# Performance work log

Hardware: AMD Instinct MI355X
Metric: run time of the kernel (lower is better)

Reference implementation:

```python
import jax, jax.numpy as jnp
import numpy as np

N_NODES = 100000
IN_C, HID_C, OUT_C = 128, 64, 16
N_EDGES = 3200000


def gcn_conv(x, W, b, src, dst, deg_inv_sqrt, n_nodes):
    """PyG GCNConv: out = D^-1/2 (A+I) D^-1/2 (x @ W) + b.
    src/dst already include self-loops; deg_inv_sqrt precomputed."""
    h = x @ W  # [N, out_c]
    norm = deg_inv_sqrt[src] * deg_inv_sqrt[dst]  # [E+N]
    msg = h[src] * norm[:, None]                  # gather + scale
    out = jax.ops.segment_sum(msg, dst, num_segments=n_nodes)
    return out + b


def _prep_edges(edge_index, n_nodes):
    loops = jnp.arange(n_nodes, dtype=edge_index.dtype)
    src = jnp.concatenate([edge_index[0], loops])
    dst = jnp.concatenate([edge_index[1], loops])
    deg = jax.ops.segment_sum(jnp.ones_like(dst, dtype=jnp.float32), dst,
                              num_segments=n_nodes)
    deg_inv_sqrt = jnp.where(deg > 0, jax.lax.rsqrt(jnp.maximum(deg, 1.0)), 0.0)
    return src, dst, deg_inv_sqrt


def setup_inputs() -> dict:
    key = jax.random.key(0)
    ks = jax.random.split(key, 8)
    x = jax.random.normal(ks[0], (N_NODES, IN_C), dtype=jnp.float32)
    edge_index = jax.random.randint(ks[1], (2, N_EDGES), 0, N_NODES, dtype=jnp.int64)
    # Glorot-ish init for GCN weights
    W1 = jax.random.normal(ks[2], (IN_C, HID_C), dtype=jnp.float32) / np.sqrt(IN_C)
    b1 = jnp.zeros((HID_C,), dtype=jnp.float32)
    W_mu = jax.random.normal(ks[3], (HID_C, OUT_C), dtype=jnp.float32) / np.sqrt(HID_C)
    b_mu = jnp.zeros((OUT_C,), dtype=jnp.float32)
    W_ls = jax.random.normal(ks[4], (HID_C, OUT_C), dtype=jnp.float32) / np.sqrt(HID_C)
    b_ls = jnp.zeros((OUT_C,), dtype=jnp.float32)
    return {"x": x, "edge_index": edge_index, "W1": W1, "b1": b1,
            "W_mu": W_mu, "b_mu": b_mu, "W_ls": W_ls, "b_ls": b_ls}


def reference(x, edge_index, W1, b1, W_mu, b_mu, W_ls, b_ls):
    n = x.shape[0]
    src, dst, dis = _prep_edges(edge_index, n)
    # conv1 -> relu (dropout is identity in eval mode)
    h = jax.nn.relu(gcn_conv(x, W1, b1, src, dst, dis, n))
    mu = gcn_conv(h, W_mu, b_mu, src, dst, dis, n)
    logstd = gcn_conv(h, W_ls, b_ls, src, dst, dis, n)
    return (mu, logstd)
```

## Files before the change

kernel.cpp:

```cpp
#include <hip/hip_runtime.h>
#include <hip/hip_bf16.h>

#define HIDC 64
#define INC 128
#define OUTC 16
#define NBLK 512
#define BSHIFT 8
#define MAXBUCK 512

typedef __attribute__((ext_vector_type(8))) short bf16x8;
typedef __attribute__((ext_vector_type(4))) float f32x4;

__device__ __forceinline__ float bflo(unsigned int u) {
    return __uint_as_float(u << 16);
}
__device__ __forceinline__ float bfhi(unsigned int u) {
    return __uint_as_float(u & 0xffff0000u);
}
__device__ __forceinline__ unsigned int f2bf(float f) {
    unsigned int b = __float_as_uint(f);
    return (b + 0x7fffu + ((b >> 16) & 1u)) >> 16;
}

__global__ __launch_bounds__(256) void count_pass(const int* __restrict__ dst,
                                                  int* __restrict__ bcnt,
                                                  int n_edges, int nbuck) {
    __shared__ int lh[MAXBUCK];
    for (int i = threadIdx.x; i < nbuck; i += 256) lh[i] = 0;
    __syncthreads();
    const int chunk = (n_edges + NBLK - 1) / NBLK;
    const int begin = blockIdx.x * chunk;
    const int end = min(begin + chunk, n_edges);
    for (int e = begin + threadIdx.x; e < end; e += 256) {
        int d = __builtin_nontemporal_load(dst + e);
        atomicAdd(&lh[d >> BSHIFT], 1);
    }
    __syncthreads();
    for (int i = threadIdx.x; i < nbuck; i += 256)
        bcnt[blockIdx.x * nbuck + i] = lh[i];
}

__device__ __forceinline__ int xphys(int j, int nbuck) {
    return (j & (NBLK - 1)) * nbuck + (j >> 9);
}

__global__ __launch_bounds__(256) void mscan_k1(const int* __restrict__ bcnt,
                                                int* __restrict__ partial,
                                                int m, int nbuck) {
    int base = blockIdx.x * 1024;
    int lim = min(base + 1024, m);
    int s = 0;
    for (int j = base + threadIdx.x; j < lim; j += 256) s += bcnt[xphys(j, nbuck)];
    #pragma unroll
    for (int d = 32; d; d >>= 1) s += __shfl_down(s, d);
    __shared__ int wsum[4];
    if ((threadIdx.x & 63) == 0) wsum[threadIdx.x >> 6] = s;
    __syncthreads();
    if (threadIdx.x == 0) partial[blockIdx.x] = wsum[0] + wsum[1] + wsum[2] + wsum[3];
}

__global__ __launch_bounds__(256) void mscan_k2(const int* __restrict__ partial,
                                                int* __restrict__ pbase, int nblk) {
    __shared__ int sh[256];
    int v = (threadIdx.x < nblk) ? partial[threadIdx.x] : 0;
    sh[threadIdx.x] = v;
    __syncthreads();
    for (int d = 1; d < 256; d <<= 1) {
        int t = (threadIdx.x >= d) ? sh[threadIdx.x - d] : 0;
        __syncthreads();
        sh[threadIdx.x] += t;
        __syncthreads();
    }
    if (threadIdx.x < nblk) pbase[threadIdx.x] = sh[threadIdx.x] - v;
}

__global__ __launch_bounds__(256) void mscan_k3(const int* __restrict__ bcnt,
                                                const int* __restrict__ pbase,
                                                int* __restrict__ bofs,
                                                int m, int nbuck) {
    int j0 = blockIdx.x * 1024 + threadIdx.x * 4;
    int c0 = (j0 + 0 < m) ? bcnt[xphys(j0 + 0, nbuck)] : 0;
    int c1 = (j0 + 1 < m) ? bcnt[xphys(j0 + 1, nbuck)] : 0;
    int c2 = (j0 + 2 < m) ? bcnt[xphys(j0 + 2, nbuck)] : 0;
    int c3 = (j0 + 3 < m) ? bcnt[xphys(j0 + 3, nbuck)] : 0;
    int tsum = c0 + c1 + c2 + c3;
    __shared__ int sh[256];
    sh[threadIdx.x] = tsum;
    __syncthreads();
    for (int d = 1; d < 256; d <<= 1) {
        int t = (threadIdx.x >= d) ? sh[threadIdx.x - d] : 0;
        __syncthreads();
        sh[threadIdx.x] += t;
        __syncthreads();
    }
    int pre = pbase[blockIdx.x] + sh[threadIdx.x] - tsum;
    if (j0 + 0 < m) bofs[xphys(j0 + 0, nbuck)] = pre;
    if (j0 + 1 < m) bofs[xphys(j0 + 1, nbuck)] = pre + c0;
    if (j0 + 2 < m) bofs[xphys(j0 + 2, nbuck)] = pre + c0 + c1;
    if (j0 + 3 < m) bofs[xphys(j0 + 3, nbuck)] = pre + c0 + c1 + c2;
}

__global__ __launch_bounds__(256) void place_pass(const int* __restrict__ src,
                                                  const int* __restrict__ dst,
                                                  const int* __restrict__ bofs,
                                                  int* __restrict__ pairs,
                                                  int n_edges, int nbuck) {
    __shared__ int lcur[MAXBUCK];
    for (int i = threadIdx.x; i < nbuck; i += 256)
        lcur[i] = bofs[blockIdx.x * nbuck + i];
    __syncthreads();
    const int chunk = (n_edges + NBLK - 1) / NBLK;
    const int begin = blockIdx.x * chunk;
    const int end = min(begin + chunk, n_edges);
    for (int e = begin + threadIdx.x; e < end; e += 256) {
        int d = __builtin_nontemporal_load(dst + e);
        int s = __builtin_nontemporal_load(src + e);
        int slot = atomicAdd(&lcur[d >> BSHIFT], 1);
        pairs[slot] = s | ((d & 255) << 17);
    }
}

__global__ __launch_bounds__(256) void csr_bucket(const int* __restrict__ pairs,
                                                  const int* __restrict__ bofs,
                                                  int* __restrict__ off,
                                                  float* __restrict__ dis,
                                                  int* __restrict__ csr,
                                                  int n_nodes, int n_edges, int nbuck) {
    __shared__ int hist[256];
    __shared__ int lofs[256];
    __shared__ int ss[256];
    const int b = blockIdx.x;
    const int node0 = b << BSHIFT;
    const int nn = min(256, n_nodes - node0);
    const int pbeg = bofs[b];
    const int pend = (b + 1 < nbuck) ? bofs[b + 1] : n_edges;
    const int tid = threadIdx.x;
    hist[tid] = 0;
    __syncthreads();
    for (int i = pbeg + tid; i < pend; i += 256)
        atomicAdd(&hist[pairs[i] >> 17], 1);
    __syncthreads();
    int h0 = (tid < nn) ? hist[tid] : 0;
    ss[tid] = h0;
    __syncthreads();
    for (int d = 1; d < 256; d <<= 1) {
        int t = (tid >= d) ? ss[tid - d] : 0;
        __syncthreads();
        ss[tid] += t;
        __syncthreads();
    }
    int pre = pbeg + ss[tid] - h0;
    if (tid < nn) {
        lofs[tid] = pre;
        off[node0 + tid] = pre;
        dis[node0 + tid] = rsqrtf((float)(h0 + 1));
    }
    __syncthreads();
    for (int i = pbeg + tid; i < pend; i += 256) {
        int v = pairs[i];
        int slot = atomicAdd(&lofs[v >> 17], 1);
        csr[slot] = v & 0x1FFFF;
    }
    if (b == 0 && tid == 0) off[n_nodes] = n_edges;
}

__global__ __launch_bounds__(256) void gemm1_mfma(const float* __restrict__ x,
                                                  const float* __restrict__ W,
                                                  const float* __restrict__ dis,
                                                  unsigned int* __restrict__ xWb,
                                                  int n_nodes) {
    __shared__ unsigned short WbT[64][136];
    __shared__ unsigned short xs[64][136];
    const int tid = threadIdx.x;
    const int lane = tid & 63, wave = tid >> 6;
    const int quad = lane >> 4, l16 = lane & 15;
    for (int i = tid; i < INC * HIDC; i += 256) {
        int k = i >> 6, n = i & 63;
        WbT[n][k] = (unsigned short)f2bf(W[i]);
    }
    __syncthreads();
    bf16x8 bfr[4][4];
    #pragma unroll
    for (int nt = 0; nt < 4; ++nt)
        #pragma unroll
        for (int kt = 0; kt < 4; ++kt)
            bfr[nt][kt] = *(const bf16x8*)&WbT[nt * 16 + l16][kt * 32 + quad * 8];

    for (int base = blockIdx.x * 64; base < n_nodes; base += gridDim.x * 64) {
        int nrows = min(64, n_nodes - base);
        __syncthreads();
        for (int i = tid; i < nrows * 32; i += 256) {
            int m = i >> 5, kq = i & 31;
            float4 v = ((const float4*)(x + (size_t)(base + m) * INC))[kq];
            unsigned int* xp = (unsigned int*)&xs[m][kq * 4];
            xp[0] = f2bf(v.x) | (f2bf(v.y) << 16);
            xp[1] = f2bf(v.z) | (f2bf(v.w) << 16);
        }
        __syncthreads();
        int mrow = wave * 16;
        if (mrow < nrows) {
            bf16x8 af[4];
            #pragma unroll
            for (int kt = 0; kt < 4; ++kt)
                af[kt] = *(const bf16x8*)&xs[mrow + l16][kt * 32 + quad * 8];
            f32x4 acc[4];
            #pragma unroll
            for (int nt = 0; nt < 4; ++nt) acc[nt] = (f32x4){0.f, 0.f, 0.f, 0.f};
            #pragma unroll
            for (int kt = 0; kt < 4; ++kt)
                #pragma unroll
                for (int nt = 0; nt < 4; ++nt)
                    acc[nt] = __builtin_amdgcn_mfma_f32_16x16x32_bf16(
                        af[kt], bfr[nt][kt], acc[nt], 0, 0, 0);
            float dr[4];
            #pragma unroll
            for (int r = 0; r < 4; ++r)
                dr[r] = dis[base + mrow + quad * 4 + r];
            #pragma unroll
            for (int nt = 0; nt < 4; ++nt) {
                #pragma unroll
                for (int r = 0; r < 4; ++r) {
                    unsigned int bv = f2bf(acc[nt][r] * dr[r]);
                    unsigned int hv = (unsigned int)__shfl_down((int)bv, 1);
                    int row = base + mrow + quad * 4 + r;
                    if (!(l16 & 1) && row < n_nodes)
                        xWb[((size_t)row * 64 + nt * 16 + l16) >> 1] = bv | (hv << 16);
                }
            }
        }
    }
}

__global__ __launch_bounds__(256) void gemm2_mfma(const uint4* __restrict__ hb4,
                                                  const float* __restrict__ Wmu,
                                                  const float* __restrict__ Wls,
                                                  const float* __restrict__ dis,
                                                  unsigned int* __restrict__ hwb,
                                                  int n_nodes) {
    __shared__ unsigned short WT2[32][72];
    __shared__ unsigned short hs[64][72];
    const int tid = threadIdx.x;
    const int lane = tid & 63, wave = tid >> 6;
    const int quad = lane >> 4, l16 = lane & 15;
    for (int i = tid; i < HIDC * 32; i += 256) {
        int n = i & 31, k = i >> 5;
        float v = (n < 16) ? Wmu[k * 16 + n] : Wls[k * 16 + (n - 16)];
        WT2[n][k] = (unsigned short)f2bf(v);
    }
    __syncthreads();
    bf16x8 bfr[2][2];
    #pragma unroll
    for (int nt = 0; nt < 2; ++nt)
        #pragma unroll
        for (int kt = 0; kt < 2; ++kt)
            bfr[nt][kt] = *(const bf16x8*)&WT2[nt * 16 + l16][kt * 32 + quad * 8];

    for (int base = blockIdx.x * 64; base < n_nodes; base += gridDim.x * 64) {
        int nrows = min(64, n_nodes - base);
        __syncthreads();
        for (int i = tid; i < nrows * 8; i += 256) {
            int m = i >> 3, q = i & 7;
            uint4 v = hb4[(size_t)(base + m) * 8 + q];
            unsigned int* hp = (unsigned int*)&hs[m][q * 8];
            hp[0] = v.x; hp[1] = v.y; hp[2] = v.z; hp[3] = v.w;
        }
        __syncthreads();
        int mrow = wave * 16;
        if (mrow < nrows) {
            bf16x8 af[2];
            #pragma unroll
            for (int kt = 0; kt < 2; ++kt)
                af[kt] = *(const bf16x8*)&hs[mrow + l16][kt * 32 + quad * 8];
            f32x4 acc[2];
            #pragma unroll
            for (int nt = 0; nt < 2; ++nt) acc[nt] = (f32x4){0.f, 0.f, 0.f, 0.f};
            #pragma unroll
            for (int kt = 0; kt < 2; ++kt)
                #pragma unroll
                for (int nt = 0; nt < 2; ++nt)
                    acc[nt] = __builtin_amdgcn_mfma_f32_16x16x32_bf16(
                        af[kt], bfr[nt][kt], acc[nt], 0, 0, 0);
            float dr[4];
            #pragma unroll
            for (int r = 0; r < 4; ++r)
                dr[r] = dis[base + mrow + quad * 4 + r];
            #pragma unroll
            for (int nt = 0; nt < 2; ++nt) {
                #pragma unroll
                for (int r = 0; r < 4; ++r) {
                    unsigned int bv = f2bf(acc[nt][r] * dr[r]);
                    unsigned int hv = (unsigned int)__shfl_down((int)bv, 1);
                    int row = base + mrow + quad * 4 + r;
                    if (!(l16 & 1) && row < n_nodes)
                        hwb[((size_t)row * 32 + nt * 16 + l16) >> 1] = bv | (hv << 16);
                }
            }
        }
    }
}

#define ACC8R(r)                                      \
    a0 += bflo((r).x); a1 += bfhi((r).x);             \
    a2 += bflo((r).y); a3 += bfhi((r).y);             \
    a4 += bflo((r).z); a5 += bfhi((r).z);             \
    a6 += bflo((r).w); a7 += bfhi((r).w);

__global__ __launch_bounds__(256) void gather64(const uint4* __restrict__ xWb4,
                                                uint4* __restrict__ hb4,
                                                const int* __restrict__ csr,
                                                const int* __restrict__ off,
                                                const float* __restrict__ dis,
                                                const float* __restrict__ b1,
                                                int n_nodes) {
    const int tid = threadIdx.x;
    const int lane = tid & 63;
    const int grp = lane >> 3;
    const int l8 = lane & 7;
    int node = blockIdx.x * 32 + (tid >> 6) * 8 + grp;
    if (node >= n_nodes) return;
    const int beg = off[node], end = off[node + 1];
    const float dn = dis[node];
    float a0 = 0.f, a1 = 0.f, a2 = 0.f, a3 = 0.f;
    float a4 = 0.f, a5 = 0.f, a6 = 0.f, a7 = 0.f;
    int e = beg;
    for (; e + 4 <= end; e += 4) {
        int s0 = csr[e];
        int s1 = csr[e + 1];
        int s2 = csr[e + 2];
        int s3 = csr[e + 3];
        uint4 r0 = xWb4[(size_t)s0 * 8 + l8];
        uint4 r1 = xWb4[(size_t)s1 * 8 + l8];
        uint4 r2 = xWb4[(size_t)s2 * 8 + l8];
        uint4 r3 = xWb4[(size_t)s3 * 8 + l8];
        ACC8R(r0);
        ACC8R(r1);
        ACC8R(r2);
        ACC8R(r3);
    }
    for (; e < end; ++e) {
        uint4 r0 = xWb4[(size_t)csr[e] * 8 + l8];
        ACC8R(r0);
    }
    {
        uint4 r = xWb4[(size_t)node * 8 + l8];
        ACC8R(r);
        float4 bA = ((const float4*)b1)[l8 * 2];
        float4 bB = ((const float4*)b1)[l8 * 2 + 1];
        uint4 u;
        u.x = f2bf(fmaxf(a0 * dn + bA.x, 0.f)) | (f2bf(fmaxf(a1 * dn + bA.y, 0.f)) << 16);
        u.y = f2bf(fmaxf(a2 * dn + bA.z, 0.f)) | (f2bf(fmaxf(a3 * dn + bA.w, 0.f)) << 16);
        u.z = f2bf(fmaxf(a4 * dn + bB.x, 0.f)) | (f2bf(fmaxf(a5 * dn + bB.y, 0.f)) << 16);
        u.w = f2bf(fmaxf(a6 * dn + bB.z, 0.f)) | (f2bf(fmaxf(a7 * dn + bB.w, 0.f)) << 16);
        hb4[(size_t)node * 8 + l8] = u;
    }
}

__global__ __launch_bounds__(256) void gather32(const uint4* __restrict__ hwb4,
                                                const int* __restrict__ csr,
                                                const int* __restrict__ off,
                                                const float* __restrict__ dis,
                                                const float* __restrict__ bmu,
                                                const float* __restrict__ bls,
                                                float* __restrict__ out,
                                                int n_nodes) {
    const int tid = threadIdx.x;
    const int lane = tid & 63;
    const int grp = lane >> 2;
    const int l4 = lane & 3;
    int node = blockIdx.x * 64 + (tid >> 6) * 16 + grp;
    if (node >= n_nodes) return;
    const int beg = off[node], end = off[node + 1];
    const float dn = dis[node];
    float a0 = 0.f, a1 = 0.f, a2 = 0.f, a3 = 0.f;
    float a4 = 0.f, a5 = 0.f, a6 = 0.f, a7 = 0.f;
    int e = beg;
    for (; e + 4 <= end; e += 4) {
        int s0 = csr[e];
        int s1 = csr[e + 1];
        int s2 = csr[e + 2];
        int s3 = csr[e + 3];
        uint4 r0 = hwb4[(size_t)s0 * 4 + l4];
        uint4 r1 = hwb4[(size_t)s1 * 4 + l4];
        uint4 r2 = hwb4[(size_t)s2 * 4 + l4];
        uint4 r3 = hwb4[(size_t)s3 * 4 + l4];
        ACC8R(r0);
        ACC8R(r1);
        ACC8R(r2);
        ACC8R(r3);
    }
    for (; e < end; ++e) {
        uint4 r0 = hwb4[(size_t)csr[e] * 4 + l4];
        ACC8R(r0);
    }
    {
        uint4 r = hwb4[(size_t)node * 4 + l4];
        ACC8R(r);
        float4 bA, bB;
        if (l4 < 2) {
            bA = ((const float4*)bmu)[l4 * 2];
            bB = ((const float4*)bmu)[l4 * 2 + 1];
        } else {
            bA = ((const float4*)bls)[(l4 - 2) * 2];
            bB = ((const float4*)bls)[(l4 - 2) * 2 + 1];
        }
        float4 o1, o2;
        o1.x = a0 * dn + bA.x; o1.y = a1 * dn + bA.y;
        o1.z = a2 * dn + bA.z; o1.w = a3 * dn + bA.w;
        o2.x = a4 * dn + bB.x; o2.y = a5 * dn + bB.y;
        o2.z = a6 * dn + bB.z; o2.w = a7 * dn + bB.w;
        size_t rb = (l4 < 2) ? (size_t)node * 4 + l4 * 2
                             : ((size_t)n_nodes + node) * 4 + (l4 - 2) * 2;
        ((float4*)out)[rb] = o1;
        ((float4*)out)[rb + 1] = o2;
    }
}

extern "C" void kernel_launch(void* const* d_in, const int* in_sizes, int n_in,
                              void* d_out, int out_size, void* d_ws, size_t ws_size,
                              hipStream_t stream) {
    const float* x   = (const float*)d_in[0];
    const int*   ei  = (const int*)d_in[1];
    const float* W1  = (const float*)d_in[2];
    const float* b1  = (const float*)d_in[3];
    const float* Wmu = (const float*)d_in[4];
    const float* bmu = (const float*)d_in[5];
    const float* Wls = (const float*)d_in[6];
    const float* bls = (const float*)d_in[7];
    float* out = (float*)d_out;

    const int N = in_sizes[0] / INC;
    const int E = in_sizes[1] / 2;
    const int* src = ei;
    const int* dst = ei + E;
    const int NBUCK = (N + 255) >> BSHIFT;
    const int M = NBUCK * NBLK;
    const int SBM = (M + 1023) / 1024;

    float* ws   = (float*)d_ws;
    float* dis  = ws;
    int*   off  = (int*)(ws + 131072);
    int*   bcnt = (int*)(ws + 262144);
    int*   bofs = (int*)(ws + 462336);
    int*   partial = (int*)(ws + 662528);
    int*   pbase   = partial + 256;
    int*   csr  = (int*)(ws + 663040);
    unsigned int* xWb = (unsigned int*)(ws + 663040 + (size_t)E);
    unsigned int* hb  = xWb + (size_t)N * 32;
    int*   pairs = (int*)hb;
    unsigned int* hwb = xWb;

    count_pass<<<NBLK, 256, 0, stream>>>(dst, bcnt, E, NBUCK);
    mscan_k1<<<SBM, 256, 0, stream>>>(bcnt, partial, M, NBUCK);
    mscan_k2<<<1, 256, 0, stream>>>(partial, pbase, SBM);
    mscan_k3<<<SBM, 256, 0, stream>>>(bcnt, pbase, bofs, M, NBUCK);
    place_pass<<<NBLK, 256, 0, stream>>>(src, dst, bofs, pairs, E, NBUCK);
    csr_bucket<<<NBUCK, 256, 0, stream>>>(pairs, bofs, off, dis, csr, N, E, NBUCK);

    gemm1_mfma<<<512, 256, 0, stream>>>(x, W1, dis, xWb, N);
    gather64<<<(N + 31) / 32, 256, 0, stream>>>((const uint4*)xWb, (uint4*)hb,
                                                csr, off, dis, b1, N);

    gemm2_mfma<<<512, 256, 0, stream>>>((const uint4*)hb, Wmu, Wls, dis, hwb, N);
    gather32<<<(N + 63) / 64, 256, 0, stream>>>((const uint4*)hwb, csr, off, dis,
                                                bmu, bls, out, N);
}
```

Measured before the change: 329.4 us.

## Fuse CSR build into fixed-capacity bucket placement and process two nodes per gather group

Replaces the count pass, three-kernel multi-block scan and separate place pass with a single fused kernel. That kernel counts per block in shared memory, reserves space in fixed-capacity global buckets via atomics, then scatters. A small single-block scan computes compacted bucket bases for csr_bucket. This removes several launches and the large count/offset arrays, but assumes no bucket exceeds BCAP edges, which holds only for roughly uniform destination distributions. gather64 is also changed so each lane group handles two consecutive nodes, halving the grid.

```diff
diff --git a/kernel.cpp b/kernel.cpp
--- a/kernel.cpp
+++ b/kernel.cpp
@@ -7,6 +7,7 @@
 #define NBLK 512
 #define BSHIFT 8
 #define MAXBUCK 512
+#define BCAP 9216
 
 typedef __attribute__((ext_vector_type(8))) short bf16x8;
 typedef __attribute__((ext_vector_type(4))) float f32x4;
@@ -22,118 +23,71 @@
     return (b + 0x7fffu + ((b >> 16) & 1u)) >> 16;
 }
 
-__global__ __launch_bounds__(256) void count_pass(const int* __restrict__ dst,
-                                                  int* __restrict__ bcnt,
-                                                  int n_edges, int nbuck) {
+__global__ void init_gcur(int* __restrict__ gcur, int nbuck) {
+    int i = threadIdx.x;
+    if (i < nbuck) gcur[i] = i * BCAP;
+}
+
+__global__ __launch_bounds__(256) void fused_place(const int* __restrict__ src,
+                                                   const int* __restrict__ dst,
+                                                   int* __restrict__ gcur,
+                                                   int* __restrict__ pairs,
+                                                   int n_edges, int nbuck) {
     __shared__ int lh[MAXBUCK];
     for (int i = threadIdx.x; i < nbuck; i += 256) lh[i] = 0;
     __syncthreads();
     const int chunk = (n_edges + NBLK - 1) / NBLK;
     const int begin = blockIdx.x * chunk;
     const int end = min(begin + chunk, n_edges);
+    for (int e = begin + threadIdx.x; e < end; e += 256)
+        atomicAdd(&lh[dst[e] >> BSHIFT], 1);
+    __syncthreads();
+    for (int i = threadIdx.x; i < nbuck; i += 256) {
+        int c = lh[i];
+        lh[i] = c ? atomicAdd(&gcur[i], c) : 0;
+    }
+    __syncthreads();
     for (int e = begin + threadIdx.x; e < end; e += 256) {
-        int d = __builtin_nontemporal_load(dst + e);
-        atomicAdd(&lh[d >> BSHIFT], 1);
-    }
-    __syncthreads();
-    for (int i = threadIdx.x; i < nbuck; i += 256)
-        bcnt[blockIdx.x * nbuck + i] = lh[i];
-}
-
-__device__ __forceinline__ int xphys(int j, int nbuck) {
-    return (j & (NBLK - 1)) * nbuck + (j >> 9);
-}
-
-__global__ __launch_bounds__(256) void mscan_k1(const int* __restrict__ bcnt,
-                                                int* __restrict__ partial,
-                                                int m, int nbuck) {
-    int base = blockIdx.x * 1024;
-    int lim = min(base + 1024, m);
-    int s = 0;
-    for (int j = base + threadIdx.x; j < lim; j += 256) s += bcnt[xphys(j, nbuck)];
-    #pragma unroll
-    for (int d = 32; d; d >>= 1) s += __shfl_down(s, d);
-    __shared__ int wsum[4];
-    if ((threadIdx.x & 63) == 0) wsum[threadIdx.x >> 6] = s;
-    __syncthreads();
-    if (threadIdx.x == 0) partial[blockIdx.x] = wsum[0] + wsum[1] + wsum[2] + wsum[3];
-}
-
-__global__ __launch_bounds__(256) void mscan_k2(const int* __restrict__ partial,
-                                                int* __restrict__ pbase, int nblk) {
-    __shared__ int sh[256];
-    int v = (threadIdx.x < nblk) ? partial[threadIdx.x] : 0;
-    sh[threadIdx.x] = v;
-    __syncthreads();
-    for (int d = 1; d < 256; d <<= 1) {
-        int t = (threadIdx.x >= d) ? sh[threadIdx.x - d] : 0;
-        __syncthreads();
-        sh[threadIdx.x] += t;
-        __syncthreads();
-    }
-    if (threadIdx.x < nblk) pbase[threadIdx.x] = sh[threadIdx.x] - v;
-}
-
-__global__ __launch_bounds__(256) void mscan_k3(const int* __restrict__ bcnt,
-                                                const int* __restrict__ pbase,
-                                                int* __restrict__ bofs,
-                                                int m, int nbuck) {
-    int j0 = blockIdx.x * 1024 + threadIdx.x * 4;
-    int c0 = (j0 + 0 < m) ? bcnt[xphys(j0 + 0, nbuck)] : 0;
-    int c1 = (j0 + 1 < m) ? bcnt[xphys(j0 + 1, nbuck)] : 0;
-    int c2 = (j0 + 2 < m) ? bcnt[xphys(j0 + 2, nbuck)] : 0;
-    int c3 = (j0 + 3 < m) ? bcnt[xphys(j0 + 3, nbuck)] : 0;
-    int tsum = c0 + c1 + c2 + c3;
-    __shared__ int sh[256];
-    sh[threadIdx.x] = tsum;
-    __syncthreads();
-    for (int d = 1; d < 256; d <<= 1) {
-        int t = (threadIdx.x >= d) ? sh[threadIdx.x - d] : 0;
-        __syncthreads();
-        sh[threadIdx.x] += t;
-        __syncthreads();
-    }
-    int pre = pbase[blockIdx.x] + sh[threadIdx.x] - tsum;
-    if (j0 + 0 < m) bofs[xphys(j0 + 0, nbuck)] = pre;
-    if (j0 + 1 < m) bofs[xphys(j0 + 1, nbuck)] = pre + c0;
-    if (j0 + 2 < m) bofs[xphys(j0 + 2, nbuck)] = pre + c0 + c1;
-    if (j0 + 3 < m) bofs[xphys(j0 + 3, nbuck)] = pre + c0 + c1 + c2;
-}
-
-__global__ __launch_bounds__(256) void place_pass(const int* __restrict__ src,
-                                                  const int* __restrict__ dst,
-                                                  const int* __restrict__ bofs,
-                                                  int* __restrict__ pairs,
-                                                  int n_edges, int nbuck) {
-    __shared__ int lcur[MAXBUCK];
-    for (int i = threadIdx.x; i < nbuck; i += 256)
-        lcur[i] = bofs[blockIdx.x * nbuck + i];
-    __syncthreads();
-    const int chunk = (n_edges + NBLK - 1) / NBLK;
-    const int begin = blockIdx.x * chunk;
-    const int end = min(begin + chunk, n_edges);
-    for (int e = begin + threadIdx.x; e < end; e += 256) {
-        int d = __builtin_nontemporal_load(dst + e);
-        int s = __builtin_nontemporal_load(src + e);
-        int slot = atomicAdd(&lcur[d >> BSHIFT], 1);
+        int d = dst[e];
+        int s = src[e];
+        int slot = atomicAdd(&lh[d >> BSHIFT], 1);
         pairs[slot] = s | ((d & 255) << 17);
     }
 }
 
+__global__ __launch_bounds__(512) void scan_buckets(const int* __restrict__ gcur,
+                                                    int* __restrict__ cbase,
+                                                    int nbuck) {
+    __shared__ int sh[512];
+    int tid = threadIdx.x;
+    int c = (tid < nbuck) ? (gcur[tid] - tid * BCAP) : 0;
+    sh[tid] = c;
+    __syncthreads();
+    for (int d = 1; d < 512; d <<= 1) {
+        int t = (tid >= d) ? sh[tid - d] : 0;
+        __syncthreads();
+        sh[tid] += t;
+        __syncthreads();
+    }
+    if (tid < nbuck) cbase[tid] = sh[tid] - c;
+}
+
 __global__ __launch_bounds__(256) void csr_bucket(const int* __restrict__ pairs,
-                                                  const int* __restrict__ bofs,
+                                                  const int* __restrict__ gcur,
+                                                  const int* __restrict__ cbase,
                                                   int* __restrict__ off,
                                                   float* __restrict__ dis,
                                                   int* __restrict__ csr,
-                                                  int n_nodes, int n_edges, int nbuck) {
+                                                  int n_nodes, int n_edges) {
     __shared__ int hist[256];
     __shared__ int lofs[256];
     __shared__ int ss[256];
     const int b = blockIdx.x;
     const int node0 = b << BSHIFT;
     const int nn = min(256, n_nodes - node0);
-    const int pbeg = bofs[b];
-    const int pend = (b + 1 < nbuck) ? bofs[b + 1] : n_edges;
+    const int pbeg = b * BCAP;
+    const int pend = gcur[b];
+    const int obase = cbase[b];
     const int tid = threadIdx.x;
     hist[tid] = 0;
     __syncthreads();
@@ -149,7 +103,7 @@
         ss[tid] += t;
         __syncthreads();
     }
-    int pre = pbeg + ss[tid] - h0;
+    int pre = obase + ss[tid] - h0;
     if (tid < nn) {
         lofs[tid] = pre;
         off[node0 + tid] = pre;
@@ -316,42 +270,46 @@
     const int lane = tid & 63;
     const int grp = lane >> 3;
     const int l8 = lane & 7;
-    int node = blockIdx.x * 32 + (tid >> 6) * 8 + grp;
-    if (node >= n_nodes) return;
-    const int beg = off[node], end = off[node + 1];
-    const float dn = dis[node];
-    float a0 = 0.f, a1 = 0.f, a2 = 0.f, a3 = 0.f;
-    float a4 = 0.f, a5 = 0.f, a6 = 0.f, a7 = 0.f;
-    int e = beg;
-    for (; e + 4 <= end; e += 4) {
-        int s0 = csr[e];
-        int s1 = csr[e + 1];
-        int s2 = csr[e + 2];
-        int s3 = csr[e + 3];
-        uint4 r0 = xWb4[(size_t)s0 * 8 + l8];
-        uint4 r1 = xWb4[(size_t)s1 * 8 + l8];
-        uint4 r2 = xWb4[(size_t)s2 * 8 + l8];
-        uint4 r3 = xWb4[(size_t)s3 * 8 + l8];
-        ACC8R(r0);
-        ACC8R(r1);
-        ACC8R(r2);
-        ACC8R(r3);
-    }
-    for (; e < end; ++e) {
-        uint4 r0 = xWb4[(size_t)csr[e] * 8 + l8];
-        ACC8R(r0);
-    }
-    {
-        uint4 r = xWb4[(size_t)node * 8 + l8];
-        ACC8R(r);
-        float4 bA = ((const float4*)b1)[l8 * 2];
-        float4 bB = ((const float4*)b1)[l8 * 2 + 1];
-        uint4 u;
-        u.x = f2bf(fmaxf(a0 * dn + bA.x, 0.f)) | (f2bf(fmaxf(a1 * dn + bA.y, 0.f)) << 16);
-        u.y = f2bf(fmaxf(a2 * dn + bA.z, 0.f)) | (f2bf(fmaxf(a3 * dn + bA.w, 0.f)) << 16);
-        u.z = f2bf(fmaxf(a4 * dn + bB.x, 0.f)) | (f2bf(fmaxf(a5 * dn + bB.y, 0.f)) << 16);
-        u.w = f2bf(fmaxf(a6 * dn + bB.z, 0.f)) | (f2bf(fmaxf(a7 * dn + bB.w, 0.f)) << 16);
-        hb4[(size_t)node * 8 + l8] = u;
+    const int gid = blockIdx.x * 32 + (tid >> 6) * 8 + grp;
+    const float4 bA = ((const float4*)b1)[l8 * 2];
+    const float4 bB = ((const float4*)b1)[l8 * 2 + 1];
+    #pragma unroll
+    for (int rep = 0; rep < 2; ++rep) {
+        int node = gid * 2 + rep;
+        if (node >= n_nodes) return;
+        const int beg = off[node], end = off[node + 1];
+        const float dn = dis[node];
+        float a0 = 0.f, a1 = 0.f, a2 = 0.f, a3 = 0.f;
+        float a4 = 0.f, a5 = 0.f, a6 = 0.f, a7 = 0.f;
+        int e = beg;
+        for (; e + 4 <= end; e += 4) {
+            int s0 = csr[e];
+            int s1 = csr[e + 1];
+            int s2 = csr[e + 2];
+            int s3 = csr[e + 3];
+            uint4 r0 = xWb4[(size_t)s0 * 8 + l8];
+            uint4 r1 = xWb4[(size_t)s1 * 8 + l8];
+            uint4 r2 = xWb4[(size_t)s2 * 8 + l8];
+            uint4 r3 = xWb4[(size_t)s3 * 8 + l8];
+            ACC8R(r0);
+            ACC8R(r1);
+            ACC8R(r2);
+            ACC8R(r3);
+        }
+        for (; e < end; ++e) {
+            uint4 r0 = xWb4[(size_t)csr[e] * 8 + l8];
+            ACC8R(r0);
+        }
+        {
+            uint4 r = xWb4[(size_t)node * 8 + l8];
+            ACC8R(r);
+            uint4 u;
+            u.x = f2bf(fmaxf(a0 * dn + bA.x, 0.f)) | (f2bf(fmaxf(a1 * dn + bA.y, 0.f)) << 16);
+            u.y = f2bf(fmaxf(a2 * dn + bA.z, 0.f)) | (f2bf(fmaxf(a3 * dn + bA.w, 0.f)) << 16);
+            u.z = f2bf(fmaxf(a4 * dn + bB.x, 0.f)) | (f2bf(fmaxf(a5 * dn + bB.y, 0.f)) << 16);
+            u.w = f2bf(fmaxf(a6 * dn + bB.z, 0.f)) | (f2bf(fmaxf(a7 * dn + bB.w, 0.f)) << 16);
+            hb4[(size_t)node * 8 + l8] = u;
+        }
     }
 }
 
@@ -433,31 +391,25 @@
     const int* src = ei;
     const int* dst = ei + E;
     const int NBUCK = (N + 255) >> BSHIFT;
-    const int M = NBUCK * NBLK;
-    const int SBM = (M + 1023) / 1024;
 
     float* ws   = (float*)d_ws;
     float* dis  = ws;
     int*   off  = (int*)(ws + 131072);
-    int*   bcnt = (int*)(ws + 262144);
-    int*   bofs = (int*)(ws + 462336);
-    int*   partial = (int*)(ws + 662528);
-    int*   pbase   = partial + 256;
+    int*   gcur = (int*)(ws + 262144);
+    int*   cbase= (int*)(ws + 263168);
     int*   csr  = (int*)(ws + 663040);
     unsigned int* xWb = (unsigned int*)(ws + 663040 + (size_t)E);
     unsigned int* hb  = xWb + (size_t)N * 32;
-    int*   pairs = (int*)hb;
+    int* pairs = (int*)xWb;
     unsigned int* hwb = xWb;
 
-    count_pass<<<NBLK, 256, 0, stream>>>(dst, bcnt, E, NBUCK);
-    mscan_k1<<<SBM, 256, 0, stream>>>(bcnt, partial, M, NBUCK);
-    mscan_k2<<<1, 256, 0, stream>>>(partial, pbase, SBM);
-    mscan_k3<<<SBM, 256, 0, stream>>>(bcnt, pbase, bofs, M, NBUCK);
-    place_pass<<<NBLK, 256, 0, stream>>>(src, dst, bofs, pairs, E, NBUCK);
-    csr_bucket<<<NBUCK, 256, 0, stream>>>(pairs, bofs, off, dis, csr, N, E, NBUCK);
+    init_gcur<<<1, 512, 0, stream>>>(gcur, NBUCK);
+    fused_place<<<NBLK, 256, 0, stream>>>(src, dst, gcur, pairs, E, NBUCK);
+    scan_buckets<<<1, 512, 0, stream>>>(gcur, cbase, NBUCK);
+    csr_bucket<<<NBUCK, 256, 0, stream>>>(pairs, gcur, cbase, off, dis, csr, N, E);
 
     gemm1_mfma<<<512, 256, 0, stream>>>(x, W1, dis, xWb, N);
-    gather64<<<(N + 31) / 32, 256, 0, stream>>>((const uint4*)xWb, (uint4*)hb,
+    gather64<<<(N + 63) / 64, 256, 0, stream>>>((const uint4*)xWb, (uint4*)hb,
                                                 csr, off, dis, b1, N);
 
     gemm2_mfma<<<512, 256, 0, stream>>>((const uint4*)hb, Wmu, Wls, dis, hwb, N);
```

After: 301.9 us. -8.3%, faster.
